# Kernel tuning notes

Measured on AMD Instinct MI355X. Metric: run time of the kernel, lower is better.

The kernel has to match this reference:

```python
import jax, jax.numpy as jnp
import numpy as np

B, H, L, F, NC, E = 512, 512, 2, 72, 10, 64
T_TRAJ, T_OUT = 120, 120
IN = F + NC * E + 1  # 713


def lstm_cell(x, h, c, Wih, Whh, bih, bhh):
    # PyTorch gate order: i, f, g, o
    gates = x @ Wih.T + bih + h @ Whh.T + bhh  # [B, 4H]
    i, f, g, o = jnp.split(gates, 4, axis=-1)
    cn = jax.nn.sigmoid(f) * c + jax.nn.sigmoid(i) * jnp.tanh(g)
    hn = jax.nn.sigmoid(o) * jnp.tanh(cn)
    return hn, cn


def _forward(src, label, class_embedding, traj, enc_emb_W, enc_emb_b, prelu_a,
             emb_W, emb_b, out_W, out_b, enc_Wih, enc_Whh, enc_bih, enc_bhh,
             dec_Wih, dec_Whh, dec_bih, dec_bhh):
    Bb = label.shape[0]
    prelu = lambda x: jnp.where(x >= 0, x, prelu_a * x)

    # --- trajectory encoder ---
    enc_in = prelu(traj @ enc_emb_W.T + enc_emb_b)  # [B, Tt, H]
    h0 = jnp.zeros((L, Bb, H), enc_in.dtype)
    c0 = jnp.zeros((L, Bb, H), enc_in.dtype)

    def enc_step(carry, x_t):
        h, c = carry
        inp = x_t
        hs, cs = [], []
        for l in range(L):
            hn, cn = lstm_cell(inp, h[l], c[l], enc_Wih[l], enc_Whh[l], enc_bih[l], enc_bhh[l])
            hs.append(hn); cs.append(cn); inp = hn
        return (jnp.stack(hs), jnp.stack(cs)), None

    (h_enc, c_enc), _ = jax.lax.scan(enc_step, (h0, c0), jnp.swapaxes(enc_in, 0, 1))

    # condition feature: outer product of label and class embedding
    cond = jnp.einsum('bi,bj->bij', label, class_embedding).reshape(Bb, -1)  # [B, NC*E]

    dec0 = jnp.zeros((Bb, F), enc_in.dtype)
    t_frac = jnp.arange(1, T_OUT + 1, dtype=enc_in.dtype) / T_OUT

    def dec_step(carry, ts):
        h, c, dec_in = carry
        gen_in = jnp.concatenate([dec_in, cond, jnp.full((Bb, 1), ts, enc_in.dtype)], axis=-1)
        x = prelu(gen_in @ emb_W.T + emb_b)  # [B, H]
        hs, cs = [], []
        for l in range(L):
            hn, cn = lstm_cell(x, h[l], c[l], dec_Wih[l], dec_Whh[l], dec_bih[l], dec_bhh[l])
            hs.append(hn); cs.append(cn); x = hn
        out = x @ out_W.T + out_b  # [B, F]
        return (jnp.stack(hs), jnp.stack(cs), out), out

    _, outs = jax.lax.scan(dec_step, (h_enc, c_enc, dec0), t_frac)
    return jnp.swapaxes(outs, 0, 1)  # [B, T_OUT, F]


def setup_inputs() -> dict:
    key = jax.random.key(0)
    ks = jax.random.split(key, 12)
    s = jnp.float32(0.04)  # ~ U(-1/sqrt(H), 1/sqrt(H)) scale
    return {
        'src': jax.random.normal(ks[0], (B, T_OUT, F), jnp.float32),
        'label': jax.random.uniform(ks[1], (B, NC), jnp.float32),
        'class_embedding': jax.random.normal(ks[2], (B, E), jnp.float32),
        'traj': jax.random.normal(ks[3], (B, T_TRAJ, 3), jnp.float32),
        'enc_emb_W': jax.random.normal(ks[4], (H, 3), jnp.float32) * s,
        'enc_emb_b': jnp.zeros((H,), jnp.float32),
        'prelu_a': jnp.full((1,), 0.25, jnp.float32),
        'emb_W': jax.random.normal(ks[5], (H, IN), jnp.float32) * s,
        'emb_b': jnp.zeros((H,), jnp.float32),
        'out_W': jax.random.normal(ks[6], (F, H), jnp.float32) * s,
        'out_b': jnp.zeros((F,), jnp.float32),
        'enc_Wih': jax.random.normal(ks[7], (L, 4 * H, H), jnp.float32) * s,
        'enc_Whh': jax.random.normal(ks[8], (L, 4 * H, H), jnp.float32) * s,
        'enc_bih': jnp.zeros((L, 4 * H), jnp.float32),
        'enc_bhh': jnp.zeros((L, 4 * H), jnp.float32),
        'dec_Wih': jax.random.normal(ks[9], (L, 4 * H, H), jnp.float32) * s,
        'dec_Whh': jax.random.normal(ks[10], (L, 4 * H, H), jnp.float32) * s,
        'dec_bih': jnp.zeros((L, 4 * H), jnp.float32),
        'dec_bhh': jnp.zeros((L, 4 * H), jnp.float32),
    }


def reference(src, label, class_embedding, traj, enc_emb_W, enc_emb_b, prelu_a,
              emb_W, emb_b, out_W, out_b, enc_Wih, enc_Whh, enc_bih, enc_bhh,
              dec_Wih, dec_Whh, dec_bih, dec_bhh):
    return _forward(src, label, class_embedding, traj, enc_emb_W, enc_emb_b, prelu_a,
                    emb_W, emb_b, out_W, out_b, enc_Wih, enc_Whh, enc_bih, enc_bhh,
                    dec_Wih, dec_Whh, dec_bih, dec_bhh)
```

## Files before the change

### kernel.cpp

```cpp
#include <hip/hip_runtime.h>
#include <math.h>

#define BB 512
#define HH 512
#define FF 72
#define NCC 10
#define EE 64
#define TTRAJ 120
#define TOUT 120
#define INWW 713
#define GG 2048
#define WSZE ((size_t)GG*1024)
#define BH  ((size_t)BB*HH)

typedef _Float16 f16x8 __attribute__((ext_vector_type(8)));
typedef float f32x4 __attribute__((ext_vector_type(4)));
typedef int i32x4 __attribute__((ext_vector_type(4)));

__device__ __forceinline__ float sigmoidf_(float x){ return 1.0f/(1.0f+__expf(-x)); }

extern "C" __device__ f32x4 llvm_amdgcn_raw_buffer_load_v4f32(
    i32x4 rsrc, int voffset, int soffset, int cpol) __asm("llvm.amdgcn.raw.buffer.load.v4f32");

__device__ __forceinline__ i32x4 make_srd(const void* p){
    union { const void* p; unsigned long long u; } a; a.p = p;
    i32x4 r;
    r.x = (int)(a.u & 0xFFFFFFFFull);
    r.y = (int)(a.u >> 32);
    r.z = -1;
    r.w = 0x00020000;
    return r;
}

__device__ __forceinline__ f16x8 ldA(i32x4 srd, int voff){
    f32x4 v = llvm_amdgcn_raw_buffer_load_v4f32(srd, voff, 0, 1);
    union { f32x4 f; f16x8 h; } u; u.f = v; return u.h;
}

__global__ void conv_wcat_kernel(const float* __restrict__ ih,
                                 const float* __restrict__ hh,
                                 _Float16* __restrict__ dst)
{
    int idx = blockIdx.x*256 + threadIdx.x;
    int j  = idx >> 8;
    int k4 = (idx & 255) * 4;
    const float* src = (k4 < 512) ? (ih + (size_t)j*512 + k4)
                                  : (hh + (size_t)j*512 + (k4-512));
    float4 v = *(const float4*)src;
    _Float16* d = dst + (size_t)j*1024 + k4;
    d[0] = (_Float16)v.x; d[1] = (_Float16)v.y;
    d[2] = (_Float16)v.z; d[3] = (_Float16)v.w;
}

__global__ void cond_kernel(const float* __restrict__ label,
                            const float* __restrict__ cemb,
                            const float* __restrict__ embW,
                            const float* __restrict__ embB,
                            float* __restrict__ cond_out)
{
    __shared__ float sl[NCC];
    __shared__ float se[EE];
    __shared__ float sc[NCC*EE];
    int b = blockIdx.x;
    int tid = threadIdx.x;
    if (tid < NCC) sl[tid] = label[b*NCC + tid];
    else if (tid >= 32 && tid < 32+EE) se[tid-32] = cemb[b*EE + (tid-32)];
    __syncthreads();
    for (int i = tid; i < NCC*EE; i += 256) sc[i] = sl[i>>6]*se[i&63];
    __syncthreads();
    for (int j = tid; j < HH; j += 256){
        const float* w = embW + (size_t)j*INWW + FF;
        float acc = embB[j];
        #pragma unroll 8
        for (int i = 0; i < NCC*EE; ++i) acc += sc[i]*w[i];
        cond_out[b*HH + j] = acc;
    }
}

__global__ void mf_kernel(const float* __restrict__ embW,
                          const float* __restrict__ outW,
                          _Float16* __restrict__ Mf)
{
    int idx = blockIdx.x*256 + threadIdx.x;
    int j = idx >> 9, k = idx & 511;
    const float* ew = embW + (size_t)j*INWW;
    float acc = 0.f;
    #pragma unroll 8
    for (int f = 0; f < FF; ++f) acc += ew[f] * outW[f*512 + k];
    Mf[idx] = (_Float16)acc;
}

__global__ void prep_kernel(const float* __restrict__ encbih, const float* __restrict__ encbhh,
                            const float* __restrict__ decbih, const float* __restrict__ decbhh,
                            const float* __restrict__ embW, const float* __restrict__ outW,
                            const float* __restrict__ outB,
                            float* __restrict__ biasC, float* __restrict__ w712,
                            float* __restrict__ constj, _Float16* __restrict__ outWf)
{
    int i = blockIdx.x*256 + threadIdx.x;
    if (i < 8192){
        int l = i >> 11, g = i & 2047;
        biasC[i] = (l < 2) ? encbih[l*GG+g] + encbhh[l*GG+g]
                           : decbih[(l-2)*GG+g] + decbhh[(l-2)*GG+g];
    } else if (i < 8704){
        int j = i - 8192;
        w712[j] = embW[(size_t)j*INWW + (INWW-1)];
    } else if (i < 9216){
        int j = i - 8704;
        float acc = 0.f;
        #pragma unroll 8
        for (int f = 0; f < FF; ++f) acc += embW[(size_t)j*INWW + f] * outB[f];
        constj[j] = acc;
    } else if (i < 9216 + 80*512){
        int ii = i - 9216;
        int f = ii >> 9, k = ii & 511;
        outWf[ii] = (f < FF) ? (_Float16)outW[f*512 + k] : (_Float16)0.f;
    }
}

__global__ __launch_bounds__(256, 1)
void persistent_kernel(const _Float16* __restrict__ wcat, const float* __restrict__ biasC,
                       const float* __restrict__ traj, const float* __restrict__ encW,
                       const float* __restrict__ encB, const float* __restrict__ prelu_a,
                       _Float16* __restrict__ xping, _Float16* __restrict__ h0p,
                       _Float16* __restrict__ h1p, _Float16* __restrict__ xdec,
                       const float* __restrict__ cond, const _Float16* __restrict__ Mf,
                       const float* __restrict__ w712, const float* __restrict__ constj,
                       const _Float16* __restrict__ outWf, const float* __restrict__ outB,
                       float* __restrict__ dout, unsigned* __restrict__ bar)
{
    __shared__ __align__(16) char smem[139776];
    float (*gx)[64][17]  = (float (*)[64][17])smem;
    float (*cst)[64][17] = (float (*)[64][17])(smem + 131072);

    const int tid = threadIdx.x;
    const int w    = tid >> 6;
    const int lane = tid & 63;
    const int m    = lane & 15;
    const int q    = lane >> 4;
    const int bid  = blockIdx.x;
    const int rt   = bid & 7;
    const int jt   = bid >> 3;
    const int r0   = rt * 64;
    const int j0   = jt * 16;
    const float pa = prelu_a[0];
    unsigned* fl = bar + rt*32*32;
    unsigned seq = 0;

    auto gbar = [&](){
        ++seq;
        __syncthreads();
        if (tid == 0)
            *(volatile unsigned*)(fl + jt*32) = seq;
        if (tid < 64){
            long long t0 = clock64();
            for(;;){
                unsigned v = (tid < 32) ? *(volatile unsigned*)(fl + tid*32) : seq;
                if (__ballot((int)(seq - v) > 0) == 0ULL) break;
                __builtin_amdgcn_s_sleep(1);
                if (clock64() - t0 > 40000000LL) break;
            }
        }
        __syncthreads();
    };

    for (int i = tid; i < 2*64*17; i += 256) ((float*)(smem + 131072))[i] = 0.f;

    f16x8 WB0[32], WB1[32];
    auto load_wb = [&](const _Float16* base0, const _Float16* base1){
        const _Float16* p0 = base0 + ((size_t)(w*512 + j0 + m))*1024 + q*8;
        const _Float16* p1 = base1 + ((size_t)(w*512 + j0 + m))*1024 + q*8;
        #pragma unroll
        for (int kc = 0; kc < 32; ++kc){
            WB0[kc] = *(const f16x8*)(p0 + kc*32);
            WB1[kc] = *(const f16x8*)(p1 + kc*32);
        }
    };

    auto stage_both = [&](const _Float16* A1, const _Float16* A2){
        i32x4 s0 = make_srd(A1), s1 = make_srd(A2);
        const int lb = lane*16;
        f16x8 va[8], vb2[8];
        #pragma unroll
        for (int i = 0; i < 8; ++i) va[i]  = ldA(s0, (r0 + i*4 + w)*1024 + lb);
        #pragma unroll
        for (int i = 0; i < 8; ++i) vb2[i] = ldA(s0, (r0 + (8+i)*4 + w)*1024 + lb);
        #pragma unroll
        for (int i = 0; i < 8; ++i){
            const int row = i*4 + w;
            *(f16x8*)(smem + row*1024 + (lb ^ ((row&7)<<4))) = va[i];
        }
        #pragma unroll
        for (int i = 0; i < 8; ++i) va[i] = ldA(s1, (r0 + i*4 + w)*1024 + lb);
        #pragma unroll
        for (int i = 0; i < 8; ++i){
            const int row = (8+i)*4 + w;
            *(f16x8*)(smem + row*1024 + (lb ^ ((row&7)<<4))) = vb2[i];
        }
        #pragma unroll
        for (int i = 0; i < 8; ++i) vb2[i] = ldA(s1, (r0 + (8+i)*4 + w)*1024 + lb);
        #pragma unroll
        for (int i = 0; i < 8; ++i){
            const int row = i*4 + w;
            *(f16x8*)(smem + 65536 + row*1024 + (lb ^ ((row&7)<<4))) = va[i];
        }
        #pragma unroll
        for (int i = 0; i < 8; ++i){
            const int row = (8+i)*4 + w;
            *(f16x8*)(smem + 65536 + row*1024 + (lb ^ ((row&7)<<4))) = vb2[i];
        }
    };

    auto layer_step = [&](const f16x8* WB, float bb, const _Float16* A1, const _Float16* A2,
                          _Float16* dst, int cidx){
        __syncthreads();
        stage_both(A1, A2);

        f32x4 acc[4];
        #pragma unroll
        for (int rf = 0; rf < 4; ++rf){ acc[rf][0]=bb; acc[rf][1]=bb; acc[rf][2]=bb; acc[rf][3]=bb; }

        const int at = m*1024 + ((q*16) ^ ((m&7)<<4));

        __syncthreads();
        const char* ab0 = (const char*)smem;
        const char* ab1 = (const char*)smem + 65536;
        #pragma unroll
        for (int kc = 0; kc < 16; ++kc){
            const int ko = at ^ (kc*64);
            #pragma unroll
            for (int rf = 0; rf < 4; ++rf){
                f16x8 av = *(const f16x8*)(ab0 + (ko + rf*16384));
                acc[rf] = __builtin_amdgcn_mfma_f32_16x16x32_f16(av, WB[kc], acc[rf], 0,0,0);
            }
        }
        #pragma unroll
        for (int kc = 0; kc < 16; ++kc){
            const int ko = at ^ (kc*64);
            #pragma unroll
            for (int rf = 0; rf < 4; ++rf){
                f16x8 av = *(const f16x8*)(ab1 + (ko + rf*16384));
                acc[rf] = __builtin_amdgcn_mfma_f32_16x16x32_f16(av, WB[16+kc], acc[rf], 0,0,0);
            }
        }
        __syncthreads();
        #pragma unroll
        for (int rf = 0; rf < 4; ++rf)
            #pragma unroll
            for (int r = 0; r < 4; ++r)
                gx[w][rf*16 + q*4 + r][m] = acc[rf][r];
        __syncthreads();
        #pragma unroll
        for (int r = 0; r < 4; ++r){
            int row = w*16 + q*4 + r;
            float ig = sigmoidf_(gx[0][row][m]);
            float fg = sigmoidf_(gx[1][row][m]);
            float gv = tanhf(gx[2][row][m]);
            float og = sigmoidf_(gx[3][row][m]);
            float cp = cst[cidx][row][m];
            float cn = fg*cp + ig*gv;
            cst[cidx][row][m] = cn;
            dst[((size_t)(r0 + row))*512 + j0 + m] = (_Float16)(og*tanhf(cn));
        }
    };

    auto gen_x = [&](int t, _Float16* xd){
        #pragma unroll
        for (int e = 0; e < 4; ++e){
            int idx = e*256 + tid;
            int row = r0 + jt*2 + (idx >> 9);
            int col = idx & 511;
            const float* tr = traj + ((size_t)row*TTRAJ + t)*3;
            const float* wv = encW + col*3;
            float v = encB[col] + tr[0]*wv[0] + tr[1]*wv[1] + tr[2]*wv[2];
            xd[(size_t)row*512 + col] = (_Float16)(v >= 0.f ? v : pa*v);
        }
    };

    auto emb_step = [&](int d, const _Float16* h1prev){
        f32x4 acc = {0.f,0.f,0.f,0.f};
        if (d > 0){
            i32x4 sh = make_srd(h1prev);
            const int vb = (r0 + w*16 + m)*1024 + q*16;
            const _Float16* bp = Mf + ((size_t)(j0 + m))*512 + q*8;
            f16x8 hv0[8], hv1[8];
            #pragma unroll
            for (int i = 0; i < 8; ++i) hv0[i] = ldA(sh, vb + i*64);
            #pragma unroll
            for (int i = 0; i < 8; ++i) hv1[i] = ldA(sh, vb + (8+i)*64);
            #pragma unroll
            for (int i = 0; i < 8; ++i)
                acc = __builtin_amdgcn_mfma_f32_16x16x32_f16(
                    hv0[i], *(const f16x8*)(bp + i*32), acc, 0,0,0);
            #pragma unroll
            for (int i = 0; i < 8; ++i)
                acc = __builtin_amdgcn_mfma_f32_16x16x32_f16(
                    hv1[i], *(const f16x8*)(bp + (8+i)*32), acc, 0,0,0);
        }
        const int col = j0 + m;
        const float ts = (float)(d+1) * (1.0f/120.0f);
        const float add = ts * w712[col] + ((d > 0) ? constj[col] : 0.f);
        #pragma unroll
        for (int r = 0; r < 4; ++r){
            int row = r0 + w*16 + q*4 + r;
            float v = acc[r] + cond[(size_t)row*512 + col] + add;
            xdec[(size_t)row*512 + col] = (_Float16)(v >= 0.f ? v : pa*v);
        }
    };

    auto out_step = [&](int dprev, const _Float16* h1v){
        if (jt >= 20 || w != 0) return;
        int b0 = r0 + (jt/5)*16;
        int f0 = (jt%5)*16;
        f32x4 acc = {0.f,0.f,0.f,0.f};
        i32x4 sh = make_srd(h1v);
        const int vb = (b0 + m)*1024 + q*16;
        const _Float16* bp = outWf + ((size_t)(f0 + m))*512 + q*8;
        f16x8 hv0[8], hv1[8];
        #pragma unroll
        for (int i = 0; i < 8; ++i) hv0[i] = ldA(sh, vb + i*64);
        #pragma unroll
        for (int i = 0; i < 8; ++i) hv1[i] = ldA(sh, vb + (8+i)*64);
        #pragma unroll
        for (int i = 0; i < 8; ++i)
            acc = __builtin_amdgcn_mfma_f32_16x16x32_f16(
                hv0[i], *(const f16x8*)(bp + i*32), acc, 0,0,0);
        #pragma unroll
        for (int i = 0; i < 8; ++i)
            acc = __builtin_amdgcn_mfma_f32_16x16x32_f16(
                hv1[i], *(const f16x8*)(bp + (8+i)*32), acc, 0,0,0);
        int f = f0 + m;
        if (f < FF){
            float ob = outB[f];
            #pragma unroll
            for (int r = 0; r < 4; ++r){
                int b = b0 + q*4 + r;
                dout[((size_t)b*TOUT + dprev)*FF + f] = acc[r] + ob;
            }
        }
    };

    load_wb(wcat + 0*WSZE, wcat + 1*WSZE);
    float bb0 = biasC[0*GG + w*512 + j0 + m];
    float bb1 = biasC[1*GG + w*512 + j0 + m];
    __syncthreads();

    gen_x(0, xping);
    gbar();

    for (int t = 0; t <= 120; ++t){
        int cur = t & 1, prv = cur ^ 1;
        if (t >= 1)
            layer_step(WB1, bb1, h0p + (size_t)prv*BH, h1p + (size_t)cur*BH, h1p + (size_t)prv*BH, 1);
        if (t < 120){
            layer_step(WB0, bb0, xping + (size_t)cur*BH, h0p + (size_t)prv*BH, h0p + (size_t)cur*BH, 0);
            if (t + 1 < 120) gen_x(t + 1, xping + (size_t)prv*BH);
        }
        gbar();
    }

    load_wb(wcat + 2*WSZE, wcat + 3*WSZE);
    bb0 = biasC[2*GG + w*512 + j0 + m];
    bb1 = biasC[3*GG + w*512 + j0 + m];

    for (int d = 0; d < 120; ++d){
        int t = 120 + d; int cur = t & 1, prv = cur ^ 1;
        emb_step(d, h1p + (size_t)prv*BH);
        if (d > 0) out_step(d - 1, h1p + (size_t)prv*BH);
        gbar();
        layer_step(WB0, bb0, xdec, h0p + (size_t)prv*BH, h0p + (size_t)cur*BH, 0);
        gbar();
        layer_step(WB1, bb1, h0p + (size_t)cur*BH, h1p + (size_t)prv*BH, h1p + (size_t)cur*BH, 1);
        gbar();
    }
    out_step(119, h1p + (size_t)1*BH);
}

extern "C" void kernel_launch(void* const* d_in, const int* in_sizes, int n_in,
                              void* d_out, int out_size, void* d_ws, size_t ws_size,
                              hipStream_t stream)
{
    (void)in_sizes; (void)n_in; (void)out_size; (void)ws_size;
    const float* label   = (const float*)d_in[1];
    const float* cemb    = (const float*)d_in[2];
    const float* traj    = (const float*)d_in[3];
    const float* encW    = (const float*)d_in[4];
    const float* encB    = (const float*)d_in[5];
    const float* prelu_a = (const float*)d_in[6];
    const float* embW    = (const float*)d_in[7];
    const float* embB    = (const float*)d_in[8];
    const float* outW    = (const float*)d_in[9];
    const float* outB    = (const float*)d_in[10];
    const float* encWih  = (const float*)d_in[11];
    const float* encWhh  = (const float*)d_in[12];
    const float* encbih  = (const float*)d_in[13];
    const float* encbhh  = (const float*)d_in[14];
    const float* decWih  = (const float*)d_in[15];
    const float* decWhh  = (const float*)d_in[16];
    const float* decbih  = (const float*)d_in[17];
    const float* decbhh  = (const float*)d_in[18];
    float* out = (float*)d_out;

    char* ws = (char*)d_ws;
    size_t off = 0;
    auto alloc = [&](size_t bytes)->char*{
        char* p = ws + off; off = (off + bytes + 255) & ~(size_t)255; return p;
    };
    _Float16* wcat  = (_Float16*)alloc(4*WSZE*2);
    _Float16* xping = (_Float16*)alloc(2*BH*2);
    _Float16* h0p   = (_Float16*)alloc(2*BH*2);
    _Float16* h1p   = (_Float16*)alloc(2*BH*2);
    _Float16* xdec  = (_Float16*)alloc(BH*2);
    float*    cond  = (float*)   alloc(BH*4);
    _Float16* Mf    = (_Float16*)alloc(512*512*2);
    _Float16* outWf = (_Float16*)alloc(80*512*2);
    float*    biasC = (float*)   alloc(4*GG*4);
    float*    w712  = (float*)   alloc(512*4);
    float*    constj= (float*)   alloc(512*4);
    unsigned* bar   = (unsigned*)alloc(8*32*32*4);

    hipMemsetAsync(h0p, 0, 4*BH*2, stream);
    hipMemsetAsync(bar, 0, 8*32*32*4, stream);

    conv_wcat_kernel<<<2048, 256, 0, stream>>>(encWih,                 encWhh,                 wcat + 0*WSZE);
    conv_wcat_kernel<<<2048, 256, 0, stream>>>(encWih + (size_t)GG*HH, encWhh + (size_t)GG*HH, wcat + 1*WSZE);
    conv_wcat_kernel<<<2048, 256, 0, stream>>>(decWih,                 decWhh,                 wcat + 2*WSZE);
    conv_wcat_kernel<<<2048, 256, 0, stream>>>(decWih + (size_t)GG*HH, decWhh + (size_t)GG*HH, wcat + 3*WSZE);
    cond_kernel<<<BB, 256, 0, stream>>>(label, cemb, embW, embB, cond);
    mf_kernel<<<1024, 256, 0, stream>>>(embW, outW, Mf);
    prep_kernel<<<197, 256, 0, stream>>>(encbih, encbhh, decbih, decbhh, embW, outW, outB,
                                         biasC, w712, constj, outWf);

    persistent_kernel<<<256, 256, 0, stream>>>(
        wcat, biasC, traj, encW, encB, prelu_a, xping, h0p, h1p, xdec,
        cond, Mf, w712, constj, outWf, outB, out, bar);
}
```

Measured before the change: 4.510 ms.

## Split global barrier and pre-stage recurrent operands to overlap loads with MFMA

After: 4.109 ms, median of 3. -8.9%, faster.

```diff
diff --git a/kernel.cpp b/kernel.cpp
--- a/kernel.cpp
+++ b/kernel.cpp
@@ -129,9 +129,11 @@
                        const _Float16* __restrict__ outWf, const float* __restrict__ outB,
                        float* __restrict__ dout, unsigned* __restrict__ bar)
 {
-    __shared__ __align__(16) char smem[139776];
-    float (*gx)[64][17]  = (float (*)[64][17])smem;
-    float (*cst)[64][17] = (float (*)[64][17])(smem + 131072);
+    __shared__ __align__(16) char smem[157184];
+    char* buf0 = smem;
+    char* buf1 = smem + 65536;
+    float (*gx)[64][17]  = (float (*)[64][17])(smem + 131072);
+    float (*cst)[64][17] = (float (*)[64][17])(smem + 148480);
 
     const int tid = threadIdx.x;
     const int w    = tid >> 6;
@@ -147,11 +149,13 @@
     unsigned* fl = bar + rt*32*32;
     unsigned seq = 0;
 
-    auto gbar = [&](){
+    auto gbar_begin = [&](){
         ++seq;
         __syncthreads();
         if (tid == 0)
             *(volatile unsigned*)(fl + jt*32) = seq;
+    };
+    auto gbar_end = [&](){
         if (tid < 64){
             long long t0 = clock64();
             for(;;){
@@ -163,8 +167,9 @@
         }
         __syncthreads();
     };
-
-    for (int i = tid; i < 2*64*17; i += 256) ((float*)(smem + 131072))[i] = 0.f;
+    auto gbar = [&](){ gbar_begin(); gbar_end(); };
+
+    for (int i = tid; i < 2*64*17; i += 256) ((float*)(smem + 148480))[i] = 0.f;
 
     f16x8 WB0[32], WB1[32];
     auto load_wb = [&](const _Float16* base0, const _Float16* base1){
@@ -177,73 +182,42 @@
         }
     };
 
-    auto stage_both = [&](const _Float16* A1, const _Float16* A2){
-        i32x4 s0 = make_srd(A1), s1 = make_srd(A2);
-        const int lb = lane*16;
-        f16x8 va[8], vb2[8];
-        #pragma unroll
-        for (int i = 0; i < 8; ++i) va[i]  = ldA(s0, (r0 + i*4 + w)*1024 + lb);
-        #pragma unroll
-        for (int i = 0; i < 8; ++i) vb2[i] = ldA(s0, (r0 + (8+i)*4 + w)*1024 + lb);
+    auto stage_rows8 = [&](i32x4 s, int g, f16x8* v){
+        #pragma unroll
+        for (int i = 0; i < 8; ++i)
+            v[i] = ldA(s, (r0 + (g*8 + i)*4 + w)*1024 + lane*16);
+    };
+    auto write_rows8 = [&](char* buf, int g, f16x8* v){
         #pragma unroll
         for (int i = 0; i < 8; ++i){
-            const int row = i*4 + w;
-            *(f16x8*)(smem + row*1024 + (lb ^ ((row&7)<<4))) = va[i];
-        }
-        #pragma unroll
-        for (int i = 0; i < 8; ++i) va[i] = ldA(s1, (r0 + i*4 + w)*1024 + lb);
-        #pragma unroll
-        for (int i = 0; i < 8; ++i){
-            const int row = (8+i)*4 + w;
-            *(f16x8*)(smem + row*1024 + (lb ^ ((row&7)<<4))) = vb2[i];
-        }
-        #pragma unroll
-        for (int i = 0; i < 8; ++i) vb2[i] = ldA(s1, (r0 + (8+i)*4 + w)*1024 + lb);
-        #pragma unroll
-        for (int i = 0; i < 8; ++i){
-            const int row = i*4 + w;
-            *(f16x8*)(smem + 65536 + row*1024 + (lb ^ ((row&7)<<4))) = va[i];
-        }
-        #pragma unroll
-        for (int i = 0; i < 8; ++i){
-            const int row = (8+i)*4 + w;
-            *(f16x8*)(smem + 65536 + row*1024 + (lb ^ ((row&7)<<4))) = vb2[i];
-        }
-    };
-
-    auto layer_step = [&](const f16x8* WB, float bb, const _Float16* A1, const _Float16* A2,
-                          _Float16* dst, int cidx){
-        __syncthreads();
-        stage_both(A1, A2);
-
-        f32x4 acc[4];
-        #pragma unroll
-        for (int rf = 0; rf < 4; ++rf){ acc[rf][0]=bb; acc[rf][1]=bb; acc[rf][2]=bb; acc[rf][3]=bb; }
-
-        const int at = m*1024 + ((q*16) ^ ((m&7)<<4));
-
-        __syncthreads();
-        const char* ab0 = (const char*)smem;
-        const char* ab1 = (const char*)smem + 65536;
-        #pragma unroll
-        for (int kc = 0; kc < 16; ++kc){
+            const int row = (g*8 + i)*4 + w;
+            *(f16x8*)(buf + row*1024 + ((lane*16) ^ ((row&7)<<4))) = v[i];
+        }
+    };
+    auto stage_avail = [&](const _Float16* A){
+        i32x4 s = make_srd(A);
+        f16x8 va[8], vb[8];
+        stage_rows8(s, 0, va);
+        stage_rows8(s, 1, vb);
+        write_rows8(buf1, 0, va);
+        write_rows8(buf1, 1, vb);
+    };
+
+    const int at = m*1024 + ((q*16) ^ ((m&7)<<4));
+
+    auto khalf = [&](const char* ab, const f16x8* WBh, int c0, int c1, f32x4* acc){
+        #pragma unroll
+        for (int kc = c0; kc < c1; ++kc){
             const int ko = at ^ (kc*64);
             #pragma unroll
             for (int rf = 0; rf < 4; ++rf){
-                f16x8 av = *(const f16x8*)(ab0 + (ko + rf*16384));
-                acc[rf] = __builtin_amdgcn_mfma_f32_16x16x32_f16(av, WB[kc], acc[rf], 0,0,0);
+                f16x8 av = *(const f16x8*)(ab + (ko + rf*16384));
+                acc[rf] = __builtin_amdgcn_mfma_f32_16x16x32_f16(av, WBh[kc], acc[rf], 0,0,0);
             }
         }
-        #pragma unroll
-        for (int kc = 0; kc < 16; ++kc){
-            const int ko = at ^ (kc*64);
-            #pragma unroll
-            for (int rf = 0; rf < 4; ++rf){
-                f16x8 av = *(const f16x8*)(ab1 + (ko + rf*16384));
-                acc[rf] = __builtin_amdgcn_mfma_f32_16x16x32_f16(av, WB[16+kc], acc[rf], 0,0,0);
-            }
-        }
-        __syncthreads();
+    };
+
+    auto elementwise = [&](f32x4* acc, _Float16* dst, int cidx){
         #pragma unroll
         for (int rf = 0; rf < 4; ++rf)
             #pragma unroll
@@ -264,6 +238,49 @@
         }
     };
 
+    auto layer_step_dec = [&](const f16x8* WB, float bb, const _Float16* Afresh,
+                              _Float16* dst, int cidx){
+        i32x4 sf = make_srd(Afresh);
+        f16x8 va[8], vb[8];
+        f32x4 acc[4];
+        #pragma unroll
+        for (int rf = 0; rf < 4; ++rf){ acc[rf][0]=bb; acc[rf][1]=bb; acc[rf][2]=bb; acc[rf][3]=bb; }
+        stage_rows8(sf, 0, va);
+        khalf(buf1, WB+16, 0, 4, acc);
+        stage_rows8(sf, 1, vb);
+        khalf(buf1, WB+16, 4, 10, acc);
+        write_rows8(buf0, 0, va);
+        khalf(buf1, WB+16, 10, 16, acc);
+        write_rows8(buf0, 1, vb);
+        __syncthreads();
+        khalf(buf0, WB, 0, 16, acc);
+        elementwise(acc, dst, cidx);
+    };
+
+    auto layer_step_enc = [&](const f16x8* WB, float bb, const _Float16* Afresh,
+                              const _Float16* Aavail, _Float16* dst, int cidx){
+        i32x4 sa = make_srd(Aavail);
+        i32x4 sf = make_srd(Afresh);
+        f16x8 va[8], vb[8];
+        stage_rows8(sa, 0, va);
+        stage_rows8(sa, 1, vb);
+        write_rows8(buf1, 0, va);
+        write_rows8(buf1, 1, vb);
+        stage_rows8(sf, 0, va);
+        __syncthreads();
+        f32x4 acc[4];
+        #pragma unroll
+        for (int rf = 0; rf < 4; ++rf){ acc[rf][0]=bb; acc[rf][1]=bb; acc[rf][2]=bb; acc[rf][3]=bb; }
+        khalf(buf1, WB+16, 0, 6, acc);
+        stage_rows8(sf, 1, vb);
+        khalf(buf1, WB+16, 6, 16, acc);
+        write_rows8(buf0, 0, va);
+        write_rows8(buf0, 1, vb);
+        __syncthreads();
+        khalf(buf0, WB, 0, 16, acc);
+        elementwise(acc, dst, cidx);
+    };
+
     auto gen_x = [&](int t, _Float16* xd){
         #pragma unroll
         for (int e = 0; e < 4; ++e){
@@ -351,9 +368,11 @@
     for (int t = 0; t <= 120; ++t){
         int cur = t & 1, prv = cur ^ 1;
         if (t >= 1)
-            layer_step(WB1, bb1, h0p + (size_t)prv*BH, h1p + (size_t)cur*BH, h1p + (size_t)prv*BH, 1);
+            layer_step_enc(WB1, bb1, h0p + (size_t)prv*BH, h1p + (size_t)cur*BH,
+                           h1p + (size_t)prv*BH, 1);
         if (t < 120){
-            layer_step(WB0, bb0, xping + (size_t)cur*BH, h0p + (size_t)prv*BH, h0p + (size_t)cur*BH, 0);
+            layer_step_enc(WB0, bb0, xping + (size_t)cur*BH, h0p + (size_t)prv*BH,
+                           h0p + (size_t)cur*BH, 0);
             if (t + 1 < 120) gen_x(t + 1, xping + (size_t)prv*BH);
         }
         gbar();
@@ -364,13 +383,16 @@
     bb1 = biasC[3*GG + w*512 + j0 + m];
 
     for (int d = 0; d < 120; ++d){
-        int t = 120 + d; int cur = t & 1, prv = cur ^ 1;
+        int cur = d & 1, prv = cur ^ 1;
         emb_step(d, h1p + (size_t)prv*BH);
         if (d > 0) out_step(d - 1, h1p + (size_t)prv*BH);
+        stage_avail(h0p + (size_t)prv*BH);
         gbar();
-        layer_step(WB0, bb0, xdec, h0p + (size_t)prv*BH, h0p + (size_t)cur*BH, 0);
-        gbar();
-        layer_step(WB1, bb1, h0p + (size_t)cur*BH, h1p + (size_t)prv*BH, h1p + (size_t)cur*BH, 1);
+        layer_step_dec(WB0, bb0, xdec, h0p + (size_t)cur*BH, 0);
+        gbar_begin();
+        stage_avail(h1p + (size_t)prv*BH);
+        gbar_end();
+        layer_step_dec(WB1, bb1, h0p + (size_t)cur*BH, h1p + (size_t)cur*BH, 1);
         gbar();
     }
     out_step(119, h1p + (size_t)1*BH);
```
